# Performance work log

Measured on AMD Instinct MI355X. Metric: run time of the kernel, lower is better.

The kernel has to match this reference:

```python
import jax, jax.numpy as jnp
import numpy as np

B = 2097152   # batch
Z = 16        # z_dim
K = 64        # num_hidden_nodes


def setup_inputs() -> dict:
    key = jax.random.key(0)
    k1, k2, k3, k4, k5 = jax.random.split(key, 5)
    return {
        "z": jax.random.normal(k1, (B, Z), dtype=jnp.float32),
        "a_0": jax.random.normal(k2, (1,), dtype=jnp.float32),
        "bk": jax.random.normal(k3, (K,), dtype=jnp.float32),
        "ck": jax.random.normal(k4, (K, Z), dtype=jnp.float32),
        "dk": jax.random.normal(k5, (K,), dtype=jnp.float32),
    }


def reference(z, a_0, bk, ck, dk):
    # Vectorized over the batch: y[b] = a_0 + sum_k bk[k] * tanh((ck @ z[b])[k] + dk[k])
    h = jnp.tanh(jnp.einsum("bz,kz->bk", z, ck) + dk)  # [B, K]
    y = a_0 + h @ bk                                     # [B]
    return y[:, None]                                     # [B, 1]
```

## Files before the change

### kernel.cpp

```cpp
#include <hip/hip_runtime.h>
#include <stdint.h>

typedef __attribute__((ext_vector_type(8)))  short  short8;
typedef __attribute__((ext_vector_type(8)))  __bf16 bf16x8;
typedef __attribute__((ext_vector_type(16))) float  floatx16;
typedef __attribute__((ext_vector_type(4)))  float  floatx4;
typedef __attribute__((ext_vector_type(2)))  float  float2v;
typedef __attribute__((ext_vector_type(4)))  uint32_t uint4v;

union Frag { short8 s; bf16x8 v; uint4v d; };
union FU   { float f; uint32_t u; };

__device__ __forceinline__ short f2bf(float f) {
    FU x; x.f = f;
    uint32_t r = x.u + 0x7fffu + ((x.u >> 16) & 1u);
    return (short)(r >> 16);
}

__device__ __forceinline__ uint32_t pack_bf2(float lo, float hi) {
    FU a, b; a.f = lo; b.f = hi;
    return __builtin_amdgcn_perm(b.u + 0x8000u, a.u + 0x8000u, 0x07060302u);
}

__device__ __forceinline__ float fexp2(float x) { return __builtin_amdgcn_exp2f(x); }
__device__ __forceinline__ float frcp(float x)  { return __builtin_amdgcn_rcpf(x); }
__device__ __forceinline__ float fclamp(float x, float lo, float hi) {
#if __has_builtin(__builtin_amdgcn_fmed3f)
    return __builtin_amdgcn_fmed3f(x, lo, hi);
#else
    return fminf(fmaxf(x, lo), hi);
#endif
}

__device__ __forceinline__ float2v tpair(float a, float b) {
    float2v t;
    t.x = fexp2(fclamp(a, -30.0f, 30.0f));
    t.y = fexp2(fclamp(b, -30.0f, 30.0f));
    return t + 1.0f;
}

__global__ __launch_bounds__(256) void mave_kernel(
    const float* __restrict__ z,
    const float* __restrict__ a0,
    const float* __restrict__ bk,
    const float* __restrict__ ck,
    const float* __restrict__ dk,
    float* __restrict__ out,
    int ntiles)
{
    const int lane = threadIdx.x & 63;
    const int m    = lane & 31;
    const int g    = lane >> 5;
    const float S  = 2.885390081777927f;

    __shared__ __align__(16) float   cinitL[2][2][16];
    __shared__ __align__(16) float2v nbL[2][2][2][4];
    __shared__ float baseL;

    if (threadIdx.x < 64) {
        const int t = threadIdx.x;
        {
            const int gg = t >> 5, hh = (t >> 4) & 1, r = t & 15;
            const int n  = (r & 3) + 8 * (r >> 2) + 4 * gg + 32 * hh;
            cinitL[gg][hh][r] = S * dk[n];
        }
        if (t < 32) {
            const int gg = t >> 4, hh = (t >> 3) & 1, rg = (t >> 2) & 1, j = t & 3;
            const int rl = 8 * rg + j,     rh = 8 * rg + 4 + j;
            const int nl = (rl & 3) + 8 * (rl >> 2) + 4 * gg + 32 * hh;
            const int nh = (rh & 3) + 8 * (rh >> 2) + 4 * gg + 32 * hh;
            float2v nb; nb.x = -2.0f * bk[nl]; nb.y = -2.0f * bk[nh];
            nbL[gg][hh][rg][j] = nb;
        }
        float bv = bk[t];
        #pragma unroll
        for (int d = 1; d < 64; d <<= 1) bv += __shfl_xor(bv, d, 64);
        if (t == 0) baseL = a0[0] + bv;
    }
    __syncthreads();

    const int wid   = (int)((blockIdx.x * blockDim.x + threadIdx.x) >> 6);
    const int tile0 = wid * 8;
    if (tile0 >= ntiles) return;
    const int tlast = ntiles - 1;

    const float* zp = z + (size_t)m * 16 + g * 8;

    floatx4 zb[3][2];
    #pragma unroll
    for (int i = 0; i < 3; ++i) {
        int ti = tile0 + i; if (ti > tlast) ti = tlast;
        const float* q = zp + (size_t)ti * 512;
        zb[i][0] = *(const floatx4*)q;
        zb[i][1] = *(const floatx4*)(q + 4);
    }

    Frag af[2];
    {
        const float* c0 = ck + m * 16 + g * 8;
        #pragma unroll
        for (int e = 0; e < 8; ++e) {
            af[0].s[e] = f2bf(c0[e] * S);
            af[1].s[e] = f2bf(c0[32 * 16 + e] * S);
        }
    }

    const floatx4* cqg = (const floatx4*)&cinitL[g][0][0];
    const floatx4* nqg = (const floatx4*)&nbL[g][0][0][0];

    float yv[8];
    #pragma unroll
    for (int i = 0; i < 8; ++i) {
        const int s3 = i % 3;

        Frag bfr;
        bfr.d[0] = pack_bf2(zb[s3][0].x, zb[s3][0].y);
        bfr.d[1] = pack_bf2(zb[s3][0].z, zb[s3][0].w);
        bfr.d[2] = pack_bf2(zb[s3][1].x, zb[s3][1].y);
        bfr.d[3] = pack_bf2(zb[s3][1].z, zb[s3][1].w);

        if (i + 3 < 8) {
            int ti = tile0 + i + 3; if (ti > tlast) ti = tlast;
            const float* q = zp + (size_t)ti * 512;
            zb[s3][0] = *(const floatx4*)q;
            zb[s3][1] = *(const floatx4*)(q + 4);
        }

        float ya = 0.0f;
        #pragma unroll
        for (int h = 0; h < 2; ++h) {
            union { floatx16 v; floatx4 q[4]; } C;
            C.q[0] = cqg[h * 4 + 0]; C.q[1] = cqg[h * 4 + 1];
            C.q[2] = cqg[h * 4 + 2]; C.q[3] = cqg[h * 4 + 3];
            floatx16 acc = __builtin_amdgcn_mfma_f32_32x32x16_bf16(
                af[h].v, bfr.v, C.v, 0, 0, 0);

            float2v Y = {0.0f, 0.0f};
            #pragma unroll
            for (int rg = 0; rg < 2; ++rg) {
                union { floatx4 q; float2v p[2]; } NA, NB;
                NA.q = nqg[h * 4 + rg * 2 + 0];
                NB.q = nqg[h * 4 + rg * 2 + 1];
                float2v T0 = tpair(acc[8 * rg + 0], acc[8 * rg + 4]);
                float2v T1 = tpair(acc[8 * rg + 1], acc[8 * rg + 5]);
                float2v T2 = tpair(acc[8 * rg + 2], acc[8 * rg + 6]);
                float2v T3 = tpair(acc[8 * rg + 3], acc[8 * rg + 7]);
                float2v P01 = T0 * T1, P23 = T2 * T3, P = P01 * P23;
                float2v R; R.x = frcp(P.x); R.y = frcp(P.y);
                float2v n01 = NA.p[0] * T1 + NA.p[1] * T0;
                float2v n23 = NB.p[0] * T3 + NB.p[1] * T2;
                float2v num = n01 * P23 + n23 * P01;
                Y += num * R;
            }
            ya += Y.x + Y.y;
        }
        yv[i] = ya;
    }

    const float base = baseL;
    float ov[8];
    #pragma unroll
    for (int i = 0; i < 8; ++i) ov[i] = __shfl_xor(yv[i], 32, 64);
    if (g == 0) {
        #pragma unroll
        for (int i = 0; i < 8; ++i) {
            int ti = tile0 + i; if (ti > tlast) ti = tlast;
            out[(size_t)ti * 32 + m] = base + yv[i] + ov[i];
        }
    }
}

extern "C" void kernel_launch(void* const* d_in, const int* in_sizes, int n_in,
                              void* d_out, int out_size, void* d_ws, size_t ws_size,
                              hipStream_t stream) {
    const float* z  = (const float*)d_in[0];
    const float* a0 = (const float*)d_in[1];
    const float* bk = (const float*)d_in[2];
    const float* ck = (const float*)d_in[3];
    const float* dk = (const float*)d_in[4];
    float* out = (float*)d_out;

    const int B      = in_sizes[0] / 16;
    const int ntiles = B / 32;

    const int blocks = (ntiles + 31) / 32;
    hipLaunchKernelGGL(mave_kernel, dim3(blocks), dim3(256), 0, stream,
                       z, a0, bk, ck, dk, out, ntiles);
}
```

Measured before the change: 200.6 us.

## Halve tiles per wave, widen tanh product tree, hoist loads before barrier

Each wave now processes 4 tiles instead of 8 with a 2-deep z prefetch, and the grid doubles in size. A launch-bounds occupancy hint of 7 is added. The tanh-sum combines 8 exp terms per reciprocal instead of 4, halving rcp count, and the clamp becomes a single fminf at 15. Global z and ck loads are issued before the shared-memory setup and barrier so their latency overlaps it. Risks: wider products may lose precision, there is more per-wave prologue overhead, and the asm trick that blocks LDS load hoisting adds extra LDS reads per tile.

```diff
diff --git a/kernel.cpp b/kernel.cpp
--- a/kernel.cpp
+++ b/kernel.cpp
@@ -24,22 +24,15 @@
 
 __device__ __forceinline__ float fexp2(float x) { return __builtin_amdgcn_exp2f(x); }
 __device__ __forceinline__ float frcp(float x)  { return __builtin_amdgcn_rcpf(x); }
-__device__ __forceinline__ float fclamp(float x, float lo, float hi) {
-#if __has_builtin(__builtin_amdgcn_fmed3f)
-    return __builtin_amdgcn_fmed3f(x, lo, hi);
-#else
-    return fminf(fmaxf(x, lo), hi);
-#endif
-}
 
 __device__ __forceinline__ float2v tpair(float a, float b) {
     float2v t;
-    t.x = fexp2(fclamp(a, -30.0f, 30.0f));
-    t.y = fexp2(fclamp(b, -30.0f, 30.0f));
+    t.x = fexp2(fminf(a, 15.0f));
+    t.y = fexp2(fminf(b, 15.0f));
     return t + 1.0f;
 }
 
-__global__ __launch_bounds__(256) void mave_kernel(
+__global__ __launch_bounds__(256, 7) void mave_kernel(
     const float* __restrict__ z,
     const float* __restrict__ a0,
     const float* __restrict__ bk,
@@ -54,41 +47,18 @@
     const float S  = 2.885390081777927f;
 
     __shared__ __align__(16) float   cinitL[2][2][16];
-    __shared__ __align__(16) float2v nbL[2][2][2][4];
+    __shared__ __align__(16) float2v nbL[2][2][8];
     __shared__ float baseL;
 
-    if (threadIdx.x < 64) {
-        const int t = threadIdx.x;
-        {
-            const int gg = t >> 5, hh = (t >> 4) & 1, r = t & 15;
-            const int n  = (r & 3) + 8 * (r >> 2) + 4 * gg + 32 * hh;
-            cinitL[gg][hh][r] = S * dk[n];
-        }
-        if (t < 32) {
-            const int gg = t >> 4, hh = (t >> 3) & 1, rg = (t >> 2) & 1, j = t & 3;
-            const int rl = 8 * rg + j,     rh = 8 * rg + 4 + j;
-            const int nl = (rl & 3) + 8 * (rl >> 2) + 4 * gg + 32 * hh;
-            const int nh = (rh & 3) + 8 * (rh >> 2) + 4 * gg + 32 * hh;
-            float2v nb; nb.x = -2.0f * bk[nl]; nb.y = -2.0f * bk[nh];
-            nbL[gg][hh][rg][j] = nb;
-        }
-        float bv = bk[t];
-        #pragma unroll
-        for (int d = 1; d < 64; d <<= 1) bv += __shfl_xor(bv, d, 64);
-        if (t == 0) baseL = a0[0] + bv;
-    }
-    __syncthreads();
-
     const int wid   = (int)((blockIdx.x * blockDim.x + threadIdx.x) >> 6);
-    const int tile0 = wid * 8;
-    if (tile0 >= ntiles) return;
+    const int tile0 = wid * 4;
     const int tlast = ntiles - 1;
 
     const float* zp = z + (size_t)m * 16 + g * 8;
 
-    floatx4 zb[3][2];
+    floatx4 zb[2][2];
     #pragma unroll
-    for (int i = 0; i < 3; ++i) {
+    for (int i = 0; i < 2; ++i) {
         int ti = tile0 + i; if (ti > tlast) ti = tlast;
         const float* q = zp + (size_t)ti * 512;
         zb[i][0] = *(const floatx4*)q;
@@ -101,69 +71,107 @@
         #pragma unroll
         for (int e = 0; e < 8; ++e) {
             af[0].s[e] = f2bf(c0[e] * S);
-            af[1].s[e] = f2bf(c0[32 * 16 + e] * S);
+            af[1].s[e] = f2bf(c0[512 + e] * S);
         }
     }
 
+    if (threadIdx.x < 64) {
+        const int t = threadIdx.x;
+        {
+            const int gg = t >> 5, hh = (t >> 4) & 1, r = t & 15;
+            const int n  = (r & 3) + 8 * (r >> 2) + 4 * gg + 32 * hh;
+            cinitL[gg][hh][r] = S * dk[n];
+        }
+        if (t < 32) {
+            const int gg = t >> 4, hh = (t >> 3) & 1, j = t & 7;
+            const int nl = (j & 3) + 8 * (j >> 2) + 4 * gg + 32 * hh;
+            float2v nb; nb.x = -2.0f * bk[nl]; nb.y = -2.0f * bk[nl + 16];
+            nbL[gg][hh][j] = nb;
+        }
+        float bv = bk[t];
+        #pragma unroll
+        for (int d = 1; d < 64; d <<= 1) bv += __shfl_xor(bv, d, 64);
+        if (t == 0) baseL = a0[0] + bv;
+    }
+    __syncthreads();
+
+    if (tile0 >= ntiles) return;
+
     const floatx4* cqg = (const floatx4*)&cinitL[g][0][0];
-    const floatx4* nqg = (const floatx4*)&nbL[g][0][0][0];
+    const floatx4* nqg = (const floatx4*)&nbL[g][0][0];
 
-    float yv[8];
+    float yv[4];
     #pragma unroll
-    for (int i = 0; i < 8; ++i) {
-        const int s3 = i % 3;
+    for (int i = 0; i < 4; ++i) {
+        Frag bfr;
+        bfr.d[0] = pack_bf2(zb[i & 1][0].x, zb[i & 1][0].y);
+        bfr.d[1] = pack_bf2(zb[i & 1][0].z, zb[i & 1][0].w);
+        bfr.d[2] = pack_bf2(zb[i & 1][1].x, zb[i & 1][1].y);
+        bfr.d[3] = pack_bf2(zb[i & 1][1].z, zb[i & 1][1].w);
 
-        Frag bfr;
-        bfr.d[0] = pack_bf2(zb[s3][0].x, zb[s3][0].y);
-        bfr.d[1] = pack_bf2(zb[s3][0].z, zb[s3][0].w);
-        bfr.d[2] = pack_bf2(zb[s3][1].x, zb[s3][1].y);
-        bfr.d[3] = pack_bf2(zb[s3][1].z, zb[s3][1].w);
+        if (i + 2 < 4) {
+            int ti = tile0 + i + 2; if (ti > tlast) ti = tlast;
+            const float* q = zp + (size_t)ti * 512;
+            zb[i & 1][0] = *(const floatx4*)q;
+            zb[i & 1][1] = *(const floatx4*)(q + 4);
+        }
 
-        if (i + 3 < 8) {
-            int ti = tile0 + i + 3; if (ti > tlast) ti = tlast;
-            const float* q = zp + (size_t)ti * 512;
-            zb[s3][0] = *(const floatx4*)q;
-            zb[s3][1] = *(const floatx4*)(q + 4);
-        }
+        int zz = 0;
+        asm volatile("" : "+v"(zz));
+        const floatx4* cq = cqg + zz;
+        const floatx4* nq = nqg + zz;
 
         float ya = 0.0f;
         #pragma unroll
         for (int h = 0; h < 2; ++h) {
             union { floatx16 v; floatx4 q[4]; } C;
-            C.q[0] = cqg[h * 4 + 0]; C.q[1] = cqg[h * 4 + 1];
-            C.q[2] = cqg[h * 4 + 2]; C.q[3] = cqg[h * 4 + 3];
+            C.q[0] = cq[h * 4 + 0]; C.q[1] = cq[h * 4 + 1];
+            C.q[2] = cq[h * 4 + 2]; C.q[3] = cq[h * 4 + 3];
             floatx16 acc = __builtin_amdgcn_mfma_f32_32x32x16_bf16(
                 af[h].v, bfr.v, C.v, 0, 0, 0);
 
-            float2v Y = {0.0f, 0.0f};
-            #pragma unroll
-            for (int rg = 0; rg < 2; ++rg) {
-                union { floatx4 q; float2v p[2]; } NA, NB;
-                NA.q = nqg[h * 4 + rg * 2 + 0];
-                NB.q = nqg[h * 4 + rg * 2 + 1];
-                float2v T0 = tpair(acc[8 * rg + 0], acc[8 * rg + 4]);
-                float2v T1 = tpair(acc[8 * rg + 1], acc[8 * rg + 5]);
-                float2v T2 = tpair(acc[8 * rg + 2], acc[8 * rg + 6]);
-                float2v T3 = tpair(acc[8 * rg + 3], acc[8 * rg + 7]);
-                float2v P01 = T0 * T1, P23 = T2 * T3, P = P01 * P23;
-                float2v R; R.x = frcp(P.x); R.y = frcp(P.y);
-                float2v n01 = NA.p[0] * T1 + NA.p[1] * T0;
-                float2v n23 = NB.p[0] * T3 + NB.p[1] * T2;
-                float2v num = n01 * P23 + n23 * P01;
-                Y += num * R;
-            }
-            ya += Y.x + Y.y;
+            union { floatx4 q; float2v p[2]; } N0, N1, N2, N3;
+            N0.q = nq[h * 4 + 0];
+            N1.q = nq[h * 4 + 1];
+            N2.q = nq[h * 4 + 2];
+            N3.q = nq[h * 4 + 3];
+
+            float2v T0 = tpair(acc[0], acc[8]);
+            float2v T1 = tpair(acc[1], acc[9]);
+            float2v P01 = T0 * T1;
+            float2v n01 = N0.p[0] * T1 + N0.p[1] * T0;
+            float2v T2 = tpair(acc[2], acc[10]);
+            float2v T3 = tpair(acc[3], acc[11]);
+            float2v P23 = T2 * T3;
+            float2v n23 = N1.p[0] * T3 + N1.p[1] * T2;
+            float2v T4 = tpair(acc[4], acc[12]);
+            float2v T5 = tpair(acc[5], acc[13]);
+            float2v P45 = T4 * T5;
+            float2v n45 = N2.p[0] * T5 + N2.p[1] * T4;
+            float2v T6 = tpair(acc[6], acc[14]);
+            float2v T7 = tpair(acc[7], acc[15]);
+            float2v P67 = T6 * T7;
+            float2v n67 = N3.p[0] * T7 + N3.p[1] * T6;
+
+            float2v PA = P01 * P23, PB = P45 * P67;
+            float2v nA = n01 * P23 + n23 * P01;
+            float2v nB = n45 * P67 + n67 * P45;
+            float2v P  = PA * PB;
+            float2v Num = nA * PB + nB * PA;
+            float2v R; R.x = frcp(P.x); R.y = frcp(P.y);
+            float2v Yh = Num * R;
+            ya += Yh.x + Yh.y;
         }
         yv[i] = ya;
     }
 
     const float base = baseL;
-    float ov[8];
+    float ov[4];
     #pragma unroll
-    for (int i = 0; i < 8; ++i) ov[i] = __shfl_xor(yv[i], 32, 64);
+    for (int i = 0; i < 4; ++i) ov[i] = __shfl_xor(yv[i], 32, 64);
     if (g == 0) {
         #pragma unroll
-        for (int i = 0; i < 8; ++i) {
+        for (int i = 0; i < 4; ++i) {
             int ti = tile0 + i; if (ti > tlast) ti = tlast;
             out[(size_t)ti * 32 + m] = base + yv[i] + ov[i];
         }
@@ -183,7 +191,7 @@
     const int B      = in_sizes[0] / 16;
     const int ntiles = B / 32;
 
-    const int blocks = (ntiles + 31) / 32;
+    const int blocks = (ntiles + 15) / 16;
     hipLaunchKernelGGL(mave_kernel, dim3(blocks), dim3(256), 0, stream,
                        z, a0, bk, ck, dk, out, ntiles);
 }
```

Result: no change. 204.4 us (+1.9%).
